# Kernel optimization log

Measured on AMD Instinct MI355X. Metric: run time of the kernel, lower is better.

The kernel has to match this reference:

```python
import jax, jax.numpy as jnp
import numpy as np

B = 128           # graphs per batch (cell.num_graphs)
N0 = 706          # genes per graph
NF = 3            # num_feature
DIM = 64          # dim_cell
LAYERS = 3        # layer_cell
VIEW_E = [2268, 6872, 3088, 3150]   # per-graph edges per view (from forward slices)
EPS = 1e-5


def _make_clusters():
    ns = [N0]
    cs = []
    for _ in range(LAYERS):
        c = np.arange(ns[-1]) // 2
        cs.append(c)
        ns.append(int(c.max()) + 1)
    return cs, ns

CLUSTERS, NS = _make_clusters()      # NS = [706, 353, 177, 89]
FINAL = NS[-1]                        # final_node


def _pool_edges(e, c):
    # PyG max_pool pool_edge: relabel by cluster, drop self-loops, coalesce
    s, d = c[e[0]], c[e[1]]
    m = s != d
    return np.unique(np.stack([s[m], d[m]]), axis=1)


def _with_self_loops(e, n):
    sl = np.arange(n, dtype=e.dtype)
    return np.concatenate([e, np.stack([sl, sl])], axis=1)


def _batch(e, n):
    off = (np.arange(B, dtype=e.dtype) * n)
    return (e[:, None, :] + off[None, :, None]).reshape(2, -1)


def setup_inputs():
    rng = np.random.default_rng(0)
    key = jax.random.key(0)
    ks = jax.random.split(key, 32)
    inp = {}
    for j, ne in enumerate(VIEW_E):
        src = rng.integers(0, N0, ne)
        dst = (src + 1 + rng.integers(0, N0 - 1, ne)) % N0
        raw = np.stack([src, dst]).astype(np.int64)
        for i in range(LAYERS):
            gat_e = _batch(_with_self_loops(raw, NS[i]), NS[i])
            inp[f"edges_v{j}_l{i}"] = jnp.asarray(gat_e, jnp.int32)
            raw = _pool_edges(raw, CLUSTERS[i])
    for i in range(LAYERS):
        cb = (CLUSTERS[i][None, :] + (np.arange(B) * NS[i + 1])[:, None]).reshape(-1)
        inp[f"cluster_l{i}"] = jnp.asarray(cb, jnp.int32)

    def nrm(k, shape, scale):
        return jax.random.normal(k, shape, jnp.float32) * scale

    inp["x"] = nrm(ks[0], (B * N0, NF), 1.0)
    dims = [NF, DIM, DIM]
    t = 1
    for i in range(LAYERS):
        inp[f"W{i}"] = nrm(ks[t], (dims[i], DIM), dims[i] ** -0.5); t += 1
        inp[f"asrc{i}"] = nrm(ks[t], (DIM,), 0.1); t += 1
        inp[f"adst{i}"] = nrm(ks[t], (DIM,), 0.1); t += 1
        inp[f"b{i}"] = jnp.zeros((DIM,), jnp.float32)
    inp["w_attn"] = nrm(ks[t], (DIM,), DIM ** -0.5); t += 1
    inp["w_lin0"] = nrm(ks[t], (4 * DIM, 4), (4 * DIM) ** -0.5); t += 1
    inp["b_lin0"] = jnp.zeros((4,), jnp.float32)
    inp["w_link0"] = nrm(ks[t], (DIM, DIM), DIM ** -0.5); t += 1
    inp["w_linkl"] = nrm(ks[t], (DIM, DIM), DIM ** -0.5); t += 1
    inp["w_link_"] = nrm(ks[t], (DIM, DIM), DIM ** -0.5); t += 1
    return inp


def _gat(x, e, W, a_s, a_d, b, n):
    # PyG GATConv, heads=1: h = xW; alpha_e = leaky_relu(a_s.h[src] + a_d.h[dst]);
    # softmax over edges per target; out = sum_e alpha * h[src] + bias
    h = x @ W
    src, dst = e[0], e[1]
    logits = jax.nn.leaky_relu(jnp.take(h @ a_s, src) + jnp.take(h @ a_d, dst), 0.2)
    m = jax.ops.segment_max(logits, dst, num_segments=n)
    p = jnp.exp(logits - jnp.take(m, dst))
    z = jax.ops.segment_sum(p, dst, num_segments=n)
    attn = p / jnp.take(z, dst)
    out = jax.ops.segment_sum(jnp.take(h, src, axis=0) * attn[:, None], dst, num_segments=n)
    return out + b


def _bn(x):
    # BatchNorm1d(affine=False), training-mode batch stats
    mu = x.mean(0)
    v = x.var(0)
    return (x - mu) * jax.lax.rsqrt(v + EPS)


def _forward(x, edges, clusters, gat_ps, w_attn, w_lin0, b_lin0, w_link0, w_linkl, w_link_):
    n_in = [B * NS[i] for i in range(LAYERS)]
    n_out = [B * NS[i + 1] for i in range(LAYERS)]
    views = []
    for j in range(4):
        h = x
        for i in range(LAYERS):
            W, a_s, a_d, bi = gat_ps[i]
            h = jax.nn.relu(_gat(h, edges[j][i], W, a_s, a_d, bi, n_in[i]))
            h = jax.ops.segment_max(h, clusters[i], num_segments=n_out[i])  # max_pool
            h = _bn(h)
        views.append(h)
    ALL = jnp.stack(views)                           # [4, M, DIM]
    Bm = jnp.einsum('vmd,d->mv', ALL, w_attn)        # linear_attn per view
    Bm = Bm / jnp.linalg.norm(Bm, axis=0, keepdims=True)
    A = jax.nn.softmax(jax.nn.leaky_relu(Bm.T @ Bm, 0.1), axis=-1)  # [4,4]
    ALLf = jnp.einsum('kmd,kl->lmd', ALL, A)         # bmm fusion
    Mn = ALLf.shape[1]
    E = ALLf.reshape(Mn, -1)                          # torch.reshape(ALL, (l,-1))
    E = E @ w_lin0 + b_lin0                           # linear_0
    w = jax.nn.softmax(E.mean(0))                     # [4]
    r = jnp.einsum('v,vmd->md', w, ALLf)
    r = jax.nn.selu(r @ w_link0)
    r = jax.nn.selu(r @ w_linkl)
    r = r @ w_link_
    return r.reshape(-1, FINAL * DIM)


def reference(x,
              edges_v0_l0, edges_v0_l1, edges_v0_l2,
              edges_v1_l0, edges_v1_l1, edges_v1_l2,
              edges_v2_l0, edges_v2_l1, edges_v2_l2,
              edges_v3_l0, edges_v3_l1, edges_v3_l2,
              cluster_l0, cluster_l1, cluster_l2,
              W0, asrc0, adst0, b0,
              W1, asrc1, adst1, b1,
              W2, asrc2, adst2, b2,
              w_attn, w_lin0, b_lin0, w_link0, w_linkl, w_link_):
    edges = [[edges_v0_l0, edges_v0_l1, edges_v0_l2],
             [edges_v1_l0, edges_v1_l1, edges_v1_l2],
             [edges_v2_l0, edges_v2_l1, edges_v2_l2],
             [edges_v3_l0, edges_v3_l1, edges_v3_l2]]
    clusters = [cluster_l0, cluster_l1, cluster_l2]
    gat_ps = [(W0, asrc0, adst0, b0), (W1, asrc1, adst1, b1), (W2, asrc2, adst2, b2)]
    return _forward(x, edges, clusters, gat_ps, w_attn, w_lin0, b_lin0,
                    w_link0, w_linkl, w_link_)
```

## Files before the change

kernel.cpp:

```cpp
#include <hip/hip_runtime.h>
#include <hip/hip_fp16.h>
#include <math.h>

#define DIM 64
#define M_FINAL (128*89)

static inline int cdiv(int a, int b) { return (a + b - 1) / b; }

__device__ inline float rdlane(float v, int l) {
    return __int_as_float(__builtin_amdgcn_readlane(__float_as_int(v), l));
}
__device__ inline unsigned packpw(float p, unsigned src) {
    return ((unsigned)__half_as_ushort(__float2half(p)) << 16) | src;
}
__device__ inline float unpackpw(unsigned ep) {
    return __half2float(__ushort_as_half((unsigned short)(ep >> 16)));
}
__device__ inline void storeval(float* p, float v) { *p = v; }
__device__ inline void storeval(__half* p, float v) { *p = __float2half(v); }

struct EdgeSets {
    const int* src[12];
    const int* dst[12];
    int ne[12];
};

struct L0Args {
    const float* x;
    __half* out[4];
    const int* rowptr[4];
    const int* colsrc[4];
    int ne[4];
    int nemax;
    double* dstats;
    const float* W;
    const float* as;
    const float* ad;
    const float* bias;
};

struct AggArgs {
    const __half* hp[4];
    void* out[4];
    const int* rowptr[4];
    const int* colsrc[4];
    int ne[4];
    int nemax;
    const float* sS;
    const float* sD;
    const float* bias;
    double* dstats;
};


__global__ void zero_kernel(float* __restrict__ p, int n) {
    int i = blockIdx.x * blockDim.x + threadIdx.x;
    if (i < n) p[i] = 0.f;
}

__global__ __launch_bounds__(768)
void csr_build_kernel(EdgeSets ES, int* __restrict__ rowptr_all,
                      int* __restrict__ colsrc_all) {
    __shared__ int cnt[768];
    __shared__ int cur[768];
    const int s = blockIdx.x;
    const int lay = s % 3;
    const int n = (lay == 0) ? 706 : (lay == 1) ? 353 : 177;
    const int ne = ES.ne[s];
    const int* __restrict__ src = ES.src[s];
    const int* __restrict__ dst = ES.dst[s];
    int* __restrict__ rowptr = rowptr_all + s * 768;
    int* __restrict__ colsrc = colsrc_all + s * 8192;
    const int t = threadIdx.x;

    cnt[t] = 0;
    __syncthreads();
    for (int k = t; k < ne; k += 768) atomicAdd(&cnt[dst[k]], 1);
    __syncthreads();
    int v = cnt[t];
    for (int off = 1; off < 768; off <<= 1) {
        int add = (t >= off) ? cnt[t - off] : 0;
        __syncthreads();
        cnt[t] += add;
        __syncthreads();
    }
    int excl = cnt[t] - v;
    if (t < n) { rowptr[t] = excl; cur[t] = excl; }
    if (t == n - 1) rowptr[n] = cnt[t];
    __syncthreads();
    for (int k = t; k < ne; k += 768) {
        int pos = atomicAdd(&cur[dst[k]], 1);
        colsrc[pos] = src[k];
    }
}

__global__ __launch_bounds__(512, 8)
void layer0_kernel(L0Args A) {
    constexpr int NPIN = 706, NPOUT = 353, HALF = 177;

    extern __shared__ char smem[];
    float* sredF = (float*)smem;
    float* fp = (float*)(smem + 4096);
    float* sSrc = fp; fp += NPIN;
    float* sDst = fp; fp += NPIN;
    float* hL4  = fp; fp += NPIN * 4;
    float* agg4 = fp; fp += 356 * 4;
    float* waL0 = fp; fp += 8;
    unsigned short* rp16 = (unsigned short*)fp;

    const int split = blockIdx.x >> 9;
    const int jg = blockIdx.x & 511;
    const int j = jg >> 7;
    const int g = jg & 127;
    const int tid = threadIdx.x;
    const int wave = tid >> 6;
    const int lane = tid & 63;

    const int n0c = split * HALF;
    const int n1c = min(NPOUT, n0c + HALF);
    const int ch0 = 2 * n0c;
    const int ch1 = 2 * n1c;

    const int* __restrict__ rowptr = A.rowptr[j];
    const int* __restrict__ colsrc = A.colsrc[j];
    const float* __restrict__ W = A.W;

    for (int k = tid; k <= NPIN; k += 512) rp16[k] = (unsigned short)rowptr[k];
    if (tid < 6) {
        int f = (tid < 3) ? tid : tid - 3;
        const float* av = (tid < 3) ? A.as : A.ad;
        float acc = 0.f;
        for (int d = 0; d < 64; ++d) acc += W[f * 64 + d] * av[d];
        waL0[tid] = acc;
    }
    __syncthreads();

    {
        const float* hb = A.x + (size_t)g * (NPIN * 3);
        for (int r = tid; r < NPIN; r += 512) {
            float h0 = hb[r * 3], h1 = hb[r * 3 + 1], h2 = hb[r * 3 + 2];
            hL4[r * 4] = h0; hL4[r * 4 + 1] = h1; hL4[r * 4 + 2] = h2; hL4[r * 4 + 3] = 0.f;
            sSrc[r] = h0 * waL0[0] + h1 * waL0[1] + h2 * waL0[2];
            sDst[r] = h0 * waL0[3] + h1 * waL0[4] + h2 * waL0[5];
        }
    }
    __syncthreads();

    const int child = ch0 + tid;
    if (child < ch1) {
        int s0 = rp16[child], e0 = rp16[child + 1];
        float sd = sDst[child];
        float m = -1e30f;
        for (int k = s0; k < e0; ++k) {
            float v = sSrc[colsrc[k]] + sd;
            v = (v >= 0.f) ? v : 0.2f * v;
            m = fmaxf(m, v);
        }
        float z = 0.f, a0 = 0.f, a1 = 0.f, a2 = 0.f;
        for (int k = s0; k < e0; ++k) {
            int sl = colsrc[k];
            float v = sSrc[sl] + sd;
            v = (v >= 0.f) ? v : 0.2f * v;
            float p = __expf(v - m);
            z += p;
            a0 += p * hL4[sl * 4];
            a1 += p * hL4[sl * 4 + 1];
            a2 += p * hL4[sl * 4 + 2];
        }
        float iz = 1.f / z;
        agg4[tid * 4]     = a0 * iz;
        agg4[tid * 4 + 1] = a1 * iz;
        agg4[tid * 4 + 2] = a2 * iz;
        agg4[tid * 4 + 3] = 0.f;
    }
    __syncthreads();

    const float w0 = W[lane], w1 = W[64 + lane], w2 = W[128 + lane];
    const float b_l = A.bias[lane];
    __half* outj = A.out[j];
    const float4* agg4v = (const float4*)agg4;
    float bs = 0.f, bs2 = 0.f;

    for (int c = n0c + wave; c < n1c; c += 8) {
        int lc = 2 * (c - n0c);
        float4 va = agg4v[lc];
        float4 vb = agg4v[lc + 1];
        float oa = va.x * w0 + va.y * w1 + va.z * w2 + b_l;
        float ob = vb.x * w0 + vb.y * w1 + vb.z * w2 + b_l;
        float vmax = fmaxf(fmaxf(oa, ob), 0.f);
        outj[((size_t)g * NPOUT + c) * 64 + lane] = __float2half(vmax);
        bs += vmax;
        bs2 += vmax * vmax;
    }
    sredF[wave * 64 + lane] = bs;
    sredF[512 + wave * 64 + lane] = bs2;
    __syncthreads();
    if (wave == 0) {
        float t1 = 0.f, t2 = 0.f;
        #pragma unroll
        for (int w = 0; w < 8; ++w) {
            t1 += sredF[w * 64 + lane];
            t2 += sredF[512 + w * 64 + lane];
        }
        atomicAdd(A.dstats + j * 128 + lane, (double)t1);
        atomicAdd(A.dstats + j * 128 + 64 + lane, (double)t2);
    }
}

__global__ void bn_finalize_kernel(const double* __restrict__ dstats,
                                   float* __restrict__ musig, int n_rows,
                                   const float* __restrict__ Wn,
                                   float* __restrict__ Wp, float* __restrict__ csh) {
    __shared__ float mur[128];
    int jv = blockIdx.x;
    int d = threadIdx.x;
    double mu = dstats[jv * 128 + d] / n_rows;
    double var = dstats[jv * 128 + 64 + d] / n_rows - mu * mu;
    float rs = rsqrtf((float)var + 1e-5f);
    musig[jv * 128 + d] = (float)mu;
    musig[jv * 128 + 64 + d] = rs;
    if (Wn != nullptr) {
        mur[d] = (float)mu; mur[64 + d] = rs;
        __syncthreads();
        float c = 0.f;
        for (int f = 0; f < 64; ++f) {
            float wp = mur[64 + f] * Wn[f * 64 + d];
            Wp[jv * 4096 + f * 64 + d] = wp;
            c += mur[f] * wp;
        }
        csh[jv * 64 + d] = c;
    }
}

__global__ __launch_bounds__(256, 5)
void proj_kernel(__half* __restrict__ buf, const float* __restrict__ Wp_all,
                 const float* __restrict__ csh_all,
                 const float* __restrict__ a_s, const float* __restrict__ a_d,
                 float* __restrict__ sS, float* __restrict__ sD, int npin) {
    const int j = blockIdx.y;
    const int lane = threadIdx.x & 63, wave = threadIdx.x >> 6;
    const int R = 128 * npin;
    const int P = R >> 1;
    __half* h = buf + (size_t)j * R * 64;
    const float* Wp = Wp_all + j * 4096;
    float Wreg[64];
    #pragma unroll
    for (int f = 0; f < 64; ++f) Wreg[f] = Wp[f * 64 + lane];
    const float cst = csh_all[j * 64 + lane];
    const float asv = a_s[lane], adv = a_d[lane];
    const int nw = gridDim.x * 4;
    for (int pr = blockIdx.x * 4 + wave; pr < P; pr += nw) {
        int r0 = pr * 2;
        float va = __half2float(h[(size_t)r0 * 64 + lane]);
        float vb = __half2float(h[(size_t)r0 * 64 + 64 + lane]);
        float o0 = 0.f, o1 = 0.f, q0 = 0.f, q1 = 0.f;
        #pragma unroll
        for (int f = 0; f < 64; f += 2) {
            o0 += rdlane(va, f)     * Wreg[f];
            q0 += rdlane(vb, f)     * Wreg[f];
            o1 += rdlane(va, f + 1) * Wreg[f + 1];
            q1 += rdlane(vb, f + 1) * Wreg[f + 1];
        }
        float oa = (o0 + o1) - cst, ob = (q0 + q1) - cst;
        h[(size_t)r0 * 64 + lane] = __float2half(oa);
        h[(size_t)r0 * 64 + 64 + lane] = __float2half(ob);
        float aa = oa * asv, da = oa * adv, ab = ob * asv, db = ob * adv;
        for (int off = 32; off > 0; off >>= 1) {
            aa += __shfl_down(aa, off, 64);
            da += __shfl_down(da, off, 64);
            ab += __shfl_down(ab, off, 64);
            db += __shfl_down(db, off, 64);
        }
        if (lane == 0) {
            sS[j * R + r0] = aa;     sD[j * R + r0] = da;
            sS[j * R + r0 + 1] = ab; sD[j * R + r0 + 1] = db;
        }
    }
}

template<int NPIN, typename OutT>
__global__ __launch_bounds__(512, 8)
void agg_kernel(AggArgs A) {
    constexpr int NPOUT = (NPIN + 1) / 2;
    constexpr int HALF = (NPOUT + 1) / 2;

    extern __shared__ char smem[];
    float* sredF = (float*)smem;
    float* fp = (float*)(smem + 4096);
    float* sSrc = fp; fp += NPIN;
    float* sDst = fp; fp += NPIN;
    unsigned* ep32 = (unsigned*)fp;
    unsigned short* rp16 = (unsigned short*)(ep32 + A.nemax);

    const int split = blockIdx.x >> 9;
    const int jg = blockIdx.x & 511;
    const int j = jg >> 7;
    const int g = jg & 127;
    const int tid = threadIdx.x;
    const int wave = tid >> 6;
    const int lane = tid & 63;

    const int n0c = split * HALF;
    const int n1c = min(NPOUT, n0c + HALF);
    const int ch0 = 2 * n0c;
    const int ch1 = min(NPIN, 2 * n1c);

    const int* __restrict__ rowptr = A.rowptr[j];
    const int* __restrict__ colsrc = A.colsrc[j];
    const int ne = A.ne[j];
    const int sbase = (j * 128 + g) * NPIN;
    const __half* __restrict__ hpg = A.hp[j] + (size_t)g * NPIN * 64 + lane;

    for (int k = tid; k <= NPIN; k += 512) rp16[k] = (unsigned short)rowptr[k];
    for (int k = tid; k < ne; k += 512) ep32[k] = (unsigned)colsrc[k];
    for (int r = tid; r < NPIN; r += 512) {
        sSrc[r] = A.sS[sbase + r];
        sDst[r] = A.sD[sbase + r];
    }
    __syncthreads();

    for (int r = ch0 + tid; r < ch1; r += 512) {
        int s0 = rp16[r], e0 = rp16[r + 1];
        float sd = sDst[r];
        float m = -1e30f, z = 0.f;
        for (int k = s0; k < e0; ++k) {
            float v = sSrc[ep32[k] & 0xFFFFu] + sd;
            v = (v >= 0.f) ? v : 0.2f * v;
            if (v > m) { z = z * __expf(m - v) + 1.f; m = v; }
            else z += __expf(v - m);
        }
        float invz = 1.f / z;
        for (int k = s0; k < e0; ++k) {
            unsigned sl = ep32[k] & 0xFFFFu;
            float v = sSrc[sl] + sd;
            v = (v >= 0.f) ? v : 0.2f * v;
            ep32[k] = packpw(__expf(v - m) * invz, sl);
        }
    }
    __syncthreads();

    const float b_l = A.bias[lane];
    OutT* outj = (OutT*)A.out[j];
    float bs = 0.f, bs2 = 0.f;

    for (int c = n0c + wave; c < n1c; c += 8) {
        float vmax = 0.f;
        #pragma unroll
        for (int ch = 0; ch < 2; ++ch) {
            int child = 2 * c + ch;
            if (child >= NPIN) break;
            int s0 = rp16[child], e0 = rp16[child + 1];
            float acc0 = 0.f, acc1 = 0.f;
            int k = s0;
            for (; k + 4 <= e0; k += 4) {
                unsigned ea = ep32[k], eb = ep32[k + 1], ec = ep32[k + 2], ed = ep32[k + 3];
                float ha = __half2float(hpg[(size_t)(ea & 0xFFFFu) << 6]);
                float hb = __half2float(hpg[(size_t)(eb & 0xFFFFu) << 6]);
                float hc = __half2float(hpg[(size_t)(ec & 0xFFFFu) << 6]);
                float hd = __half2float(hpg[(size_t)(ed & 0xFFFFu) << 6]);
                acc0 += unpackpw(ea) * ha + unpackpw(eb) * hb;
                acc1 += unpackpw(ec) * hc + unpackpw(ed) * hd;
            }
            for (; k < e0; ++k) {
                unsigned ea = ep32[k];
                acc0 += unpackpw(ea) * __half2float(hpg[(size_t)(ea & 0xFFFFu) << 6]);
            }
            float o = acc0 + acc1 + b_l;
            vmax = fmaxf(vmax, fmaxf(o, 0.f));
        }
        storeval(&outj[((size_t)g * NPOUT + c) * 64 + lane], vmax);
        bs += vmax;
        bs2 += vmax * vmax;
    }
    sredF[wave * 64 + lane] = bs;
    sredF[512 + wave * 64 + lane] = bs2;
    __syncthreads();
    if (wave == 0) {
        float t1 = 0.f, t2 = 0.f;
        #pragma unroll
        for (int w = 0; w < 8; ++w) {
            t1 += sredF[w * 64 + lane];
            t2 += sredF[512 + w * 64 + lane];
        }
        atomicAdd(A.dstats + j * 128 + lane, (double)t1);
        atomicAdd(A.dstats + j * 128 + 64 + lane, (double)t2);
    }
}

__global__ __launch_bounds__(256)
void head_reduce_kernel(const float* __restrict__ ALL, const float* __restrict__ musig,
                        const float* __restrict__ w_attn,
                        float* __restrict__ S, float* __restrict__ cm) {
    __shared__ float S_loc[16];
    __shared__ float cm_loc[256];
    const int t = threadIdx.x, wave = t >> 6, lane = t & 63;
    if (t < 16) S_loc[t] = 0.f;
    cm_loc[t] = 0.f;
    __syncthreads();
    const float wa = w_attn[lane];
    float cacc[4] = {0.f, 0.f, 0.f, 0.f};
    for (int m = blockIdx.x * 4 + wave; m < M_FINAL; m += gridDim.x * 4) {
        float b4[4];
        float csum = 0.f;
        #pragma unroll
        for (int v = 0; v < 4; ++v) {
            float val = (ALL[((size_t)v * M_FINAL + m) * 64 + lane] - musig[v * 128 + lane])
                        * musig[v * 128 + 64 + lane];
            csum += val;
            float p = val * wa;
            for (int off = 32; off > 0; off >>= 1) p += __shfl_down(p, off, 64);
            b4[v] = __shfl(p, 0, 64);
        }
        cacc[m & 3] += csum;
        if (lane < 16) atomicAdd(&S_loc[lane], b4[lane >> 2] * b4[lane & 3]);
    }
    #pragma unroll
    for (int q = 0; q < 4; ++q) atomicAdd(&cm_loc[q * 64 + lane], cacc[q]);
    __syncthreads();
    if (t < 16) atomicAdd(&S[t], S_loc[t]);
    atomicAdd(&cm[t], cm_loc[t]);
}

__global__ void fuse_small_kernel(const float* __restrict__ S, const float* __restrict__ cm,
                                  const float* __restrict__ w_lin0, const float* __restrict__ b_lin0,
                                  float* __restrict__ cvec) {
    const int lane = threadIdx.x;
    float pa0 = 0.f, pa1 = 0.f, pa2 = 0.f, pa3 = 0.f;
    #pragma unroll
    for (int q = 0; q < 4; ++q) {
        int c = q * 64 + lane;
        float cmv = cm[c] / (float)M_FINAL;
        pa0 += cmv * w_lin0[c * 4 + 0];
        pa1 += cmv * w_lin0[c * 4 + 1];
        pa2 += cmv * w_lin0[c * 4 + 2];
        pa3 += cmv * w_lin0[c * 4 + 3];
    }
    for (int off = 32; off > 0; off >>= 1) {
        pa0 += __shfl_down(pa0, off, 64);
        pa1 += __shfl_down(pa1, off, 64);
        pa2 += __shfl_down(pa2, off, 64);
        pa3 += __shfl_down(pa3, off, 64);
    }
    if (lane != 0) return;
    float e4[4] = {pa0 + b_lin0[0], pa1 + b_lin0[1], pa2 + b_lin0[2], pa3 + b_lin0[3]};
    float cn[4];
    for (int v = 0; v < 4; ++v) cn[v] = sqrtf(S[v * 4 + v]);
    float A[16];
    for (int u = 0; u < 4; ++u) {
        float row[4]; float mx = -1e30f;
        for (int v = 0; v < 4; ++v) {
            float g = S[u * 4 + v] / (cn[u] * cn[v]);
            g = (g >= 0.f) ? g : 0.1f * g;
            row[v] = g; mx = fmaxf(mx, g);
        }
        float sum = 0.f;
        for (int v = 0; v < 4; ++v) { row[v] = expf(row[v] - mx); sum += row[v]; }
        for (int v = 0; v < 4; ++v) A[u * 4 + v] = row[v] / sum;
    }
    float mx = fmaxf(fmaxf(e4[0], e4[1]), fmaxf(e4[2], e4[3]));
    float sum = 0.f, w[4];
    for (int v = 0; v < 4; ++v) { w[v] = expf(e4[v] - mx); sum += w[v]; }
    for (int v = 0; v < 4; ++v) w[v] /= sum;
    for (int k = 0; k < 4; ++k) {
        float c = 0.f;
        for (int v = 0; v < 4; ++v) c += A[k * 4 + v] * w[v];
        cvec[k] = c;
    }
}

__global__ __launch_bounds__(256)
void head_out_kernel(const float* __restrict__ ALL, const float* __restrict__ musig,
                     const float* __restrict__ cvec,
                     const float* __restrict__ W0, const float* __restrict__ W1,
                     const float* __restrict__ W2, float* __restrict__ outp) {
    __shared__ float Wl[3][64 * 64];
    const int t = threadIdx.x, wave = t >> 6, lane = t & 63;
    for (int k = t; k < 4096; k += 256) {
        Wl[0][k] = W0[k]; Wl[1][k] = W1[k]; Wl[2][k] = W2[k];
    }
    __syncthreads();
    const float c0 = cvec[0], c1 = cvec[1], c2 = cvec[2], c3 = cvec[3];
    const float scale = 1.0507009873554805f;
    const float alpha = 1.6732632423543772f;
    for (int m = blockIdx.x * 4 + wave; m < M_FINAL; m += gridDim.x * 4) {
        float r =
            c0 * ((ALL[((size_t)0 * M_FINAL + m) * 64 + lane] - musig[0 * 128 + lane]) * musig[0 * 128 + 64 + lane]) +
            c1 * ((ALL[((size_t)1 * M_FINAL + m) * 64 + lane] - musig[1 * 128 + lane]) * musig[1 * 128 + 64 + lane]) +
            c2 * ((ALL[((size_t)2 * M_FINAL + m) * 64 + lane] - musig[2 * 128 + lane]) * musig[2 * 128 + 64 + lane]) +
            c3 * ((ALL[((size_t)3 * M_FINAL + m) * 64 + lane] - musig[3 * 128 + lane]) * musig[3 * 128 + 64 + lane]);
        #pragma unroll
        for (int s = 0; s < 3; ++s) {
            float o0 = 0.f, o1 = 0.f, o2 = 0.f, o3 = 0.f;
            #pragma unroll
            for (int f = 0; f < 64; f += 4) {
                o0 += rdlane(r, f)     * Wl[s][f * 64 + lane];
                o1 += rdlane(r, f + 1) * Wl[s][(f + 1) * 64 + lane];
                o2 += rdlane(r, f + 2) * Wl[s][(f + 2) * 64 + lane];
                o3 += rdlane(r, f + 3) * Wl[s][(f + 3) * 64 + lane];
            }
            float o = (o0 + o1) + (o2 + o3);
            if (s < 2) o = (o > 0.f) ? scale * o : scale * alpha * expm1f(o);
            r = o;
        }
        outp[(size_t)m * 64 + lane] = r;
    }
}

extern "C" void kernel_launch(void* const* d_in, const int* in_sizes, int n_in,
                              void* d_out, int out_size, void* d_ws, size_t ws_size,
                              hipStream_t stream) {
    const float* x = (const float*)d_in[15];

    float* ws = (float*)d_ws;
    double* dstats_all = (double*)ws;
    float*  cm         = ws + 3072;
    float*  S          = ws + 3328;
    float*  cvec       = ws + 3344;
    float*  musig_all  = ws + 3584;
    float*  Wp_all     = ws + 5120;
    float*  csh_all    = ws + 37888;
    int*    rowptr_all = (int*)(ws + 38400);
    int*    colsrc_all = (int*)(ws + 47616);
    float*  sS1        = ws + 145920;
    float*  sD1        = sS1 + 180736;
    float*  sS2        = sD1 + 180736;
    float*  sD2        = sS2 + 90624;
    __half* A16        = (__half*)(sD2 + 90624);
    __half* B16        = (__half*)((float*)A16 + 5783552);
    float*  ALLb       = (float*)B16 + 2899968;
    const size_t as0h = (size_t)128 * 353 * 64;
    const size_t as1h = (size_t)128 * 177 * 64;

    EdgeSets ES;
    int nemax[3] = {0, 0, 0};
    for (int s = 0; s < 12; ++s) {
        const int* e = (const int*)d_in[s];
        int E = in_sizes[s] / 2;
        ES.src[s] = e;
        ES.dst[s] = e + E;
        ES.ne[s] = E / 128;
        int lay = s % 3;
        if (ES.ne[s] > nemax[lay]) nemax[lay] = ES.ne[s];
    }

    int SM0 = 4096 + (706 * 6 + 356 * 4 + 8) * 4 + 708 * 2;
    SM0 = (SM0 + 15) & ~15;
    int SMa1 = 4096 + (2 * 353) * 4 + nemax[1] * 4 + 355 * 2;
    SMa1 = (SMa1 + 15) & ~15;
    int SMa2 = 4096 + (2 * 177) * 4 + nemax[2] * 4 + 179 * 2;
    SMa2 = (SMa2 + 15) & ~15;
    (void)hipFuncSetAttribute(reinterpret_cast<const void*>(&layer0_kernel),
                              hipFuncAttributeMaxDynamicSharedMemorySize, SM0);
    (void)hipFuncSetAttribute(reinterpret_cast<const void*>(&agg_kernel<353, __half>),
                              hipFuncAttributeMaxDynamicSharedMemorySize, SMa1);
    (void)hipFuncSetAttribute(reinterpret_cast<const void*>(&agg_kernel<177, float>),
                              hipFuncAttributeMaxDynamicSharedMemorySize, SMa2);

    zero_kernel<<<cdiv(3584, 256), 256, 0, stream>>>(ws, 3584);
    csr_build_kernel<<<12, 768, 0, stream>>>(ES, rowptr_all, colsrc_all);

    {
        L0Args A;
        A.x = x;
        for (int j = 0; j < 4; ++j) {
            int s = j * 3;
            A.rowptr[j] = rowptr_all + s * 768;
            A.colsrc[j] = colsrc_all + s * 8192;
            A.ne[j] = ES.ne[s];
            A.out[j] = A16 + j * as0h;
        }
        A.nemax = nemax[0];
        A.dstats = dstats_all;
        A.W = (const float*)d_in[16];
        A.as = (const float*)d_in[17];
        A.ad = (const float*)d_in[18];
        A.bias = (const float*)d_in[19];
        layer0_kernel<<<1024, 512, SM0, stream>>>(A);
    }
    bn_finalize_kernel<<<4, 64, 0, stream>>>(dstats_all, musig_all, 128 * 353,
                                             (const float*)d_in[20], Wp_all, csh_all);

    proj_kernel<<<dim3(320, 4), 256, 0, stream>>>(A16, Wp_all, csh_all,
                                                  (const float*)d_in[21], (const float*)d_in[22],
                                                  sS1, sD1, 353);
    {
        AggArgs A;
        for (int j = 0; j < 4; ++j) {
            int s = j * 3 + 1;
            A.rowptr[j] = rowptr_all + s * 768;
            A.colsrc[j] = colsrc_all + s * 8192;
            A.ne[j] = ES.ne[s];
            A.hp[j] = A16 + j * as0h;
            A.out[j] = B16 + j * as1h;
        }
        A.nemax = nemax[1];
        A.sS = sS1; A.sD = sD1;
        A.bias = (const float*)d_in[23];
        A.dstats = dstats_all + 512;
        agg_kernel<353, __half><<<1024, 512, SMa1, stream>>>(A);
    }
    bn_finalize_kernel<<<4, 64, 0, stream>>>(dstats_all + 512, musig_all + 512, 128 * 177,
                                             (const float*)d_in[24], Wp_all + 16384, csh_all + 256);

    proj_kernel<<<dim3(320, 4), 256, 0, stream>>>(B16, Wp_all + 16384, csh_all + 256,
                                                  (const float*)d_in[25], (const float*)d_in[26],
                                                  sS2, sD2, 177);
    {
        AggArgs A;
        for (int j = 0; j < 4; ++j) {
            int s = j * 3 + 2;
            A.rowptr[j] = rowptr_all + s * 768;
            A.colsrc[j] = colsrc_all + s * 8192;
            A.ne[j] = ES.ne[s];
            A.hp[j] = B16 + j * as1h;
            A.out[j] = ALLb + (size_t)j * M_FINAL * 64;
        }
        A.nemax = nemax[2];
        A.sS = sS2; A.sD = sD2;
        A.bias = (const float*)d_in[27];
        A.dstats = dstats_all + 1024;
        agg_kernel<177, float><<<1024, 512, SMa2, stream>>>(A);
    }
    bn_finalize_kernel<<<4, 64, 0, stream>>>(dstats_all + 1024, musig_all + 1024, 128 * 89,
                                             nullptr, nullptr, nullptr);

    const float* musig2 = musig_all + 1024;
    head_reduce_kernel<<<256, 256, 0, stream>>>(ALLb, musig2, (const float*)d_in[28], S, cm);
    fuse_small_kernel<<<1, 64, 0, stream>>>(S, cm, (const float*)d_in[29], (const float*)d_in[30], cvec);
    head_out_kernel<<<256, 256, 0, stream>>>(ALLb, musig2, cvec,
                                             (const float*)d_in[31], (const float*)d_in[32],
                                             (const float*)d_in[33], (float*)d_out);
}
```

Before: 416.4 us.

## Use MFMA f16 matrix instructions for per-view GAT projection in proj_kernel

Rewrites the projection kernel to compute 16-row tiles with __builtin_amdgcn_mfma_f32_16x16x32_f16, staging the transposed weight matrix in shared memory as fp16. This replaces the per-lane readlane/FMA scalar dot products, which were issue-bound. Attention-score reductions now use xor-shuffles across 16 lanes. The weights are rounded to fp16 (they were fp32 before), which may change precision slightly. Occupancy and grid size are also reduced.

```diff
diff --git a/kernel.cpp b/kernel.cpp
--- a/kernel.cpp
+++ b/kernel.cpp
@@ -6,6 +6,9 @@
 #define M_FINAL (128*89)
 
 static inline int cdiv(int a, int b) { return (a + b - 1) / b; }
+
+typedef _Float16 v8h __attribute__((ext_vector_type(8)));
+typedef float v4f __attribute__((ext_vector_type(4)));
 
 __device__ inline float rdlane(float v, int l) {
     return __int_as_float(__builtin_amdgcn_readlane(__float_as_int(v), l));
@@ -232,48 +235,80 @@
     }
 }
 
-__global__ __launch_bounds__(256, 5)
+__global__ __launch_bounds__(256, 4)
 void proj_kernel(__half* __restrict__ buf, const float* __restrict__ Wp_all,
                  const float* __restrict__ csh_all,
                  const float* __restrict__ a_s, const float* __restrict__ a_d,
                  float* __restrict__ sS, float* __restrict__ sD, int npin) {
+    __shared__ _Float16 Wt[64 * 64];
     const int j = blockIdx.y;
-    const int lane = threadIdx.x & 63, wave = threadIdx.x >> 6;
+    const int tid = threadIdx.x;
+    const int lane = tid & 63, wave = tid >> 6;
+    const int lc = lane & 15, quad = lane >> 4;
     const int R = 128 * npin;
-    const int P = R >> 1;
     __half* h = buf + (size_t)j * R * 64;
     const float* Wp = Wp_all + j * 4096;
-    float Wreg[64];
+
+    for (int k = tid; k < 4096; k += 256) {
+        int f = k >> 6, d = k & 63;
+        Wt[d * 64 + f] = (_Float16)Wp[k];
+    }
+    __syncthreads();
+
+    v8h bfrag[4][2];
     #pragma unroll
-    for (int f = 0; f < 64; ++f) Wreg[f] = Wp[f * 64 + lane];
-    const float cst = csh_all[j * 64 + lane];
-    const float asv = a_s[lane], adv = a_d[lane];
-    const int nw = gridDim.x * 4;
-    for (int pr = blockIdx.x * 4 + wave; pr < P; pr += nw) {
-        int r0 = pr * 2;
-        float va = __half2float(h[(size_t)r0 * 64 + lane]);
-        float vb = __half2float(h[(size_t)r0 * 64 + 64 + lane]);
-        float o0 = 0.f, o1 = 0.f, q0 = 0.f, q1 = 0.f;
-        #pragma unroll
-        for (int f = 0; f < 64; f += 2) {
-            o0 += rdlane(va, f)     * Wreg[f];
-            q0 += rdlane(vb, f)     * Wreg[f];
-            o1 += rdlane(va, f + 1) * Wreg[f + 1];
-            q1 += rdlane(vb, f + 1) * Wreg[f + 1];
-        }
-        float oa = (o0 + o1) - cst, ob = (q0 + q1) - cst;
-        h[(size_t)r0 * 64 + lane] = __float2half(oa);
-        h[(size_t)r0 * 64 + 64 + lane] = __float2half(ob);
-        float aa = oa * asv, da = oa * adv, ab = ob * asv, db = ob * adv;
-        for (int off = 32; off > 0; off >>= 1) {
-            aa += __shfl_down(aa, off, 64);
-            da += __shfl_down(da, off, 64);
-            ab += __shfl_down(ab, off, 64);
-            db += __shfl_down(db, off, 64);
-        }
-        if (lane == 0) {
-            sS[j * R + r0] = aa;     sD[j * R + r0] = da;
-            sS[j * R + r0 + 1] = ab; sD[j * R + r0 + 1] = db;
+    for (int t = 0; t < 4; ++t)
+        #pragma unroll
+        for (int s = 0; s < 2; ++s)
+            bfrag[t][s] = *(const v8h*)&Wt[(t * 16 + lc) * 64 + s * 32 + quad * 8];
+
+    float cshv[4], asv[4], adv[4];
+    #pragma unroll
+    for (int t = 0; t < 4; ++t) {
+        cshv[t] = csh_all[j * 64 + t * 16 + lc];
+        asv[t] = a_s[t * 16 + lc];
+        adv[t] = a_d[t * 16 + lc];
+    }
+
+    const int ntiles = R >> 4;
+    for (int tile = blockIdx.x * 4 + wave; tile < ntiles; tile += gridDim.x * 4) {
+        const int rowbase = tile * 16;
+        const __half* arow = h + ((size_t)(rowbase + lc)) * 64 + quad * 8;
+        v8h a0 = *(const v8h*)arow;
+        v8h a1 = *(const v8h*)(arow + 32);
+        v4f acc[4];
+        #pragma unroll
+        for (int t = 0; t < 4; ++t) {
+            acc[t] = (v4f){0.f, 0.f, 0.f, 0.f};
+            acc[t] = __builtin_amdgcn_mfma_f32_16x16x32_f16(a0, bfrag[t][0], acc[t], 0, 0, 0);
+            acc[t] = __builtin_amdgcn_mfma_f32_16x16x32_f16(a1, bfrag[t][1], acc[t], 0, 0, 0);
+        }
+        float pS[4] = {0.f, 0.f, 0.f, 0.f};
+        float pD[4] = {0.f, 0.f, 0.f, 0.f};
+        #pragma unroll
+        for (int t = 0; t < 4; ++t) {
+            #pragma unroll
+            for (int r = 0; r < 4; ++r) {
+                float o = acc[t][r] - cshv[t];
+                h[((size_t)(rowbase + quad * 4 + r)) * 64 + t * 16 + lc] = __float2half(o);
+                pS[r] += o * asv[t];
+                pD[r] += o * adv[t];
+            }
+        }
+        #pragma unroll
+        for (int m = 1; m < 16; m <<= 1) {
+            #pragma unroll
+            for (int r = 0; r < 4; ++r) {
+                pS[r] += __shfl_xor(pS[r], m, 64);
+                pD[r] += __shfl_xor(pD[r], m, 64);
+            }
+        }
+        if (lc == 0) {
+            #pragma unroll
+            for (int r = 0; r < 4; ++r) {
+                sS[j * R + rowbase + quad * 4 + r] = pS[r];
+                sD[j * R + rowbase + quad * 4 + r] = pD[r];
+            }
         }
     }
 }
@@ -580,7 +615,7 @@
     bn_finalize_kernel<<<4, 64, 0, stream>>>(dstats_all, musig_all, 128 * 353,
                                              (const float*)d_in[20], Wp_all, csh_all);
 
-    proj_kernel<<<dim3(320, 4), 256, 0, stream>>>(A16, Wp_all, csh_all,
+    proj_kernel<<<dim3(256, 4), 256, 0, stream>>>(A16, Wp_all, csh_all,
                                                   (const float*)d_in[21], (const float*)d_in[22],
                                                   sS1, sD1, 353);
     {
@@ -602,7 +637,7 @@
     bn_finalize_kernel<<<4, 64, 0, stream>>>(dstats_all + 512, musig_all + 512, 128 * 177,
                                              (const float*)d_in[24], Wp_all + 16384, csh_all + 256);
 
-    proj_kernel<<<dim3(320, 4), 256, 0, stream>>>(B16, Wp_all + 16384, csh_all + 256,
+    proj_kernel<<<dim3(256, 4), 256, 0, stream>>>(B16, Wp_all + 16384, csh_all + 256,
                                                   (const float*)d_in[25], (const float*)d_in[26],
                                                   sS2, sD2, 177);
     {
```

Measured after the change: 355.7 us. 14.6% less time.
